# Kernel optimization log

Hardware: AMD Instinct MI355X
Metric: run time of the kernel (lower is better)

## Reference

```python
import jax, jax.numpy as jnp
import numpy as np

# EdMIPS quantizer constants for 2-bit
HWGQ_STEP = 0.538      # hwgq_steps[2]
GAUSS_STEP = 0.996     # gaussian_steps[2]
ABIT = 2
WBIT = 2
BN_EPS = 1e-3


def setup_inputs() -> dict:
    key = jax.random.key(0)
    k1, k2 = jax.random.split(key, 2)
    x = jax.random.normal(k1, (32, 128, 56, 56), jnp.float32)
    gamma = jnp.ones((128,), jnp.float32)
    beta = jnp.zeros((128,), jnp.float32)
    weight = jax.random.normal(k2, (128, 128, 3, 3), jnp.float32) * 0.05
    return {"x": x, "gamma": gamma, "beta": beta, "weight": weight}


def _hwgq(x):
    # HWGQ: clamp to [0, step*(2^abit - 1)], then round to uniform levels.
    lvls = float(2 ** ABIT - 1)
    thr = HWGQ_STEP * lvls
    y = jnp.clip(x, 0.0, thr)
    q = jnp.round(y / HWGQ_STEP) * HWGQ_STEP
    # straight-through estimator: forward = q, backward = d/dy (clip mask)
    return y + jax.lax.stop_gradient(q - y)


def _gauss_quantize(w):
    # step scaled by weight std (detached, torch uses .item()); mid-rise quantizer.
    step = GAUSS_STEP * jax.lax.stop_gradient(jnp.std(w))
    lvls = float(2 ** WBIT) / 2.0
    q = (jnp.round(w / step + 0.5) - 0.5) * step
    thr = (lvls - 0.5) * step
    q = jnp.clip(q, -thr, thr)
    # full straight-through: backward = identity
    return w + jax.lax.stop_gradient(q - w)


def reference(x, gamma, beta, weight):
    # BatchNorm2d (training-mode batch stats, biased variance, eps=0.001)
    mean = jnp.mean(x, axis=(0, 2, 3), keepdims=True)
    var = jnp.var(x, axis=(0, 2, 3), keepdims=True)
    xn = (x - mean) * jax.lax.rsqrt(var + BN_EPS)
    xn = xn * gamma[None, :, None, None] + beta[None, :, None, None]
    # quantized activations and weights, then plain conv (bias=False)
    a = _hwgq(xn)
    qw = _gauss_quantize(weight)
    out = jax.lax.conv_general_dilated(
        a, qw,
        window_strides=(1, 1),
        padding=((1, 1), (1, 1)),
        dimension_numbers=("NCHW", "OIHW", "NCHW"),
    )
    return out  # [32, 128, 56, 56]
```

## Files before the change

kernel.cpp:

```cpp
#include <hip/hip_runtime.h>

typedef int i32x4 __attribute__((ext_vector_type(4)));

#define C_IN 128
#define HW 56
#define PIX 3136
#define NPLANE 401408
#define PROWB 7424
#define APAD_NSTRIDE 430592

static __device__ __forceinline__ void gload_lds16(const void* g, void* l) {
  __builtin_amdgcn_global_load_lds((__attribute__((address_space(1))) unsigned int*)g,
                                   (__attribute__((address_space(3))) unsigned int*)l, 16, 0, 0);
}

__global__ __launch_bounds__(256) void bn_partial_k(const float* __restrict__ x,
                                                    double* __restrict__ part) {
  const int c = blockIdx.x, sl = blockIdx.y;
  const int tid = threadIdx.x;
  double s = 0.0, s2 = 0.0;
  for (int n = sl * 4; n < sl * 4 + 4; ++n) {
    const float4* p = (const float4*)(x + (size_t)(n * C_IN + c) * PIX);
    for (int i = tid; i < PIX / 4; i += 256) {
      float4 v = p[i];
      s  += (double)v.x + (double)v.y + (double)v.z + (double)v.w;
      s2 += (double)v.x * v.x + (double)v.y * v.y + (double)v.z * v.z + (double)v.w * v.w;
    }
  }
  __shared__ double red[8];
  const int lane = tid & 63, wv = tid >> 6;
  for (int off = 32; off; off >>= 1) { s += __shfl_down(s, off); s2 += __shfl_down(s2, off); }
  if (lane == 0) { red[wv * 2] = s; red[wv * 2 + 1] = s2; }
  __syncthreads();
  if (tid == 0) {
    part[(c * 8 + sl) * 2] = red[0] + red[2] + red[4] + red[6];
    part[(c * 8 + sl) * 2 + 1] = red[1] + red[3] + red[5] + red[7];
  }
}

__global__ __launch_bounds__(256) void w_partial_k(const float* __restrict__ w,
                                                   double* __restrict__ part) {
  const int b = blockIdx.x, tid = threadIdx.x;
  double s = 0.0, s2 = 0.0;
  const float4* p = (const float4*)w;
  for (int i = b * 576 + tid; i < (b + 1) * 576; i += 256) {
    float4 v = p[i];
    s  += (double)v.x + (double)v.y + (double)v.z + (double)v.w;
    s2 += (double)v.x * v.x + (double)v.y * v.y + (double)v.z * v.z + (double)v.w * v.w;
  }
  __shared__ double red[8];
  const int lane = tid & 63, wv = tid >> 6;
  for (int off = 32; off; off >>= 1) { s += __shfl_down(s, off); s2 += __shfl_down(s2, off); }
  if (lane == 0) { red[wv * 2] = s; red[wv * 2 + 1] = s2; }
  __syncthreads();
  if (tid == 0) {
    part[b * 2] = red[0] + red[2] + red[4] + red[6];
    part[b * 2 + 1] = red[1] + red[3] + red[5] + red[7];
  }
}

__global__ __launch_bounds__(256) void quant_act_k(const float* __restrict__ x,
                                                   const double* __restrict__ bnpart,
                                                   const float* __restrict__ gamma,
                                                   const float* __restrict__ beta,
                                                   signed char* __restrict__ apad) {
  const int hh = blockIdx.x;
  const int n = blockIdx.y;
  const int tid = threadIdx.x;
  __shared__ float2 aff[128];
  __shared__ __align__(16) signed char lds[58 * 144];
  if (tid < 128) {
    double s = 0.0, s2 = 0.0;
    for (int i = 0; i < 8; ++i) { s += bnpart[(tid * 8 + i) * 2]; s2 += bnpart[(tid * 8 + i) * 2 + 1]; }
    const double mean = s / 100352.0;
    const double var = s2 / 100352.0 - mean * mean;
    const double inv = 1.0 / sqrt(var + 1e-3);
    aff[tid] = make_float2((float)((double)gamma[tid] * inv),
                           (float)((double)beta[tid] - mean * inv * (double)gamma[tid]));
  }
  uint4* lds4 = (uint4*)lds;
  for (int i = tid; i < 58 * 144 / 16; i += 256) lds4[i] = make_uint4(0, 0, 0, 0);
  __syncthreads();
  if (hh >= 1 && hh <= 56) {
    const float* xp = x + (size_t)n * NPLANE + (hh - 1) * HW;
    for (int i = tid; i < C_IN * HW; i += 256) {
      const int w = i % HW, c = i / HW;
      const float v = xp[(size_t)c * PIX + w];
      const float2 af = aff[c];
      const float xn = fmaf(v, af.x, af.y);
      const float y = fminf(fmaxf(xn, 0.f), 1.614f);
      lds[(w + 1) * 144 + c] = (signed char)(int)rintf(y * (1.f / 0.538f));
    }
  }
  __syncthreads();
  signed char* dst = apad + (size_t)n * APAD_NSTRIDE;
  for (int i = tid; i < 58 * 8; i += 256) {
    const int col = i >> 3, c16 = i & 7;
    const int pp = hh * 58 + col;
    *(uint4*)(dst + (((size_t)pp * 128 + c16 * 16) ^ ((pp & 7) << 4))) = lds4[col * 9 + c16];
  }
}

__global__ __launch_bounds__(128) void quant_w_k(const float* __restrict__ w,
                                                 const double* __restrict__ wpart,
                                                 signed char* __restrict__ wq,
                                                 float* __restrict__ stepp) {
  const int oc = blockIdx.x, tid = threadIdx.x;
  __shared__ float steps;
  __shared__ __align__(16) signed char lds[9 * 128];
  if (tid < 64) {
    double s = wpart[tid * 2], s2 = wpart[tid * 2 + 1];
    for (int off = 32; off; off >>= 1) { s += __shfl_down(s, off); s2 += __shfl_down(s2, off); }
    if (tid == 0) {
      const double mean = s / 147456.0;
      const double var = s2 / 147456.0 - mean * mean;
      steps = 0.996f * (float)sqrt(var);
      if (oc == 0) stepp[0] = steps;
    }
  }
  __syncthreads();
  const float step = steps;
  for (int i = tid; i < 1152; i += 128) {
    const int c = i / 9, rs = i % 9;
    const float v = w[(size_t)(oc * C_IN + c) * 9 + rs];
    float t = 2.f * rintf(v / step + 0.5f) - 1.f;
    t = fminf(fmaxf(t, -3.f), 3.f);
    lds[rs * 128 + c] = (signed char)(int)t;
  }
  __syncthreads();
  for (int i = tid; i < 72; i += 128) {
    const int rs = i >> 3, c16 = i & 7;
    *(uint4*)(wq + rs * 16384 + ((oc * 128 + c16 * 16) ^ ((oc & 7) << 4))) =
        *(const uint4*)(lds + rs * 128 + c16 * 16);
  }
}

__global__ __launch_bounds__(256, 2) void conv_k(const signed char* __restrict__ apad,
                                                 const signed char* __restrict__ wq,
                                                 const float* __restrict__ stepp,
                                                 float* __restrict__ out) {
  __shared__ __align__(16) signed char Al[45056];
  __shared__ __align__(16) signed char Wl[2][16384];
  const int rg = blockIdx.x;
  const int n = blockIdx.y;
  const int tid = threadIdx.x;
  const int wv = tid >> 6, lane = tid & 63;
  const int lr = lane & 15, q4 = lane >> 4;
  const int kq = q4 * 16;
  const int ohalf = (wv & 1) * 64;
  const int phalf = (wv >> 1) * 112;

  {
    const signed char* gsrc = apad + (size_t)n * APAD_NSTRIDE + (size_t)(rg * 4) * PROWB;
    for (int i = wv; i < 44; i += 4)
      gload_lds16(gsrc + i * 1024 + lane * 16, Al + i * 1024);
  }
  for (int i = wv; i < 16; i += 4)
    gload_lds16(wq + i * 1024 + lane * 16, &Wl[0][i * 1024]);

  int pbase[7];
#pragma unroll
  for (int pf = 0; pf < 7; ++pf) {
    const int po = phalf + pf * 16 + lr;
    pbase[7 > pf ? pf : 0] = (po / 56) * 58 + po % 56;
  }

  i32x4 acc[7][4];
#pragma unroll
  for (int i = 0; i < 7; ++i)
#pragma unroll
    for (int j = 0; j < 4; ++j) acc[i][j] = (i32x4){0, 0, 0, 0};

  __syncthreads();

  for (int rs = 0; rs < 9; ++rs) {
    if (rs < 8) {
      for (int i = wv; i < 16; i += 4)
        gload_lds16(wq + (rs + 1) * 16384 + i * 1024 + lane * 16, &Wl[(rs + 1) & 1][i * 1024]);
    }
    const int r = rs / 3, s = rs - 3 * r;
    const int poff = r * 58 + s;
    const signed char* Wb = Wl[rs & 1];
#pragma unroll
    for (int k64 = 0; k64 < 2; ++k64) {
      const int kb = k64 * 64 + kq;
      i32x4 wf[4];
#pragma unroll
      for (int of = 0; of < 4; ++of) {
        const int row = ohalf + of * 16 + lr;
        wf[of] = *(const i32x4*)(Wb + row * 128 + (kb ^ ((row & 7) << 4)));
      }
#pragma unroll
      for (int pf = 0; pf < 7; ++pf) {
        const int p = pbase[pf] + poff;
        const i32x4 bf = *(const i32x4*)(Al + p * 128 + (kb ^ ((p & 7) << 4)));
        acc[pf][0] = __builtin_amdgcn_mfma_i32_16x16x64_i8(wf[0], bf, acc[pf][0], 0, 0, 0);
        acc[pf][1] = __builtin_amdgcn_mfma_i32_16x16x64_i8(wf[1], bf, acc[pf][1], 0, 0, 0);
        acc[pf][2] = __builtin_amdgcn_mfma_i32_16x16x64_i8(wf[2], bf, acc[pf][2], 0, 0, 0);
        acc[pf][3] = __builtin_amdgcn_mfma_i32_16x16x64_i8(wf[3], bf, acc[pf][3], 0, 0, 0);
      }
    }
    __syncthreads();
  }

  const float oscale = 0.269f * stepp[0];
  float* outn = out + (size_t)n * NPLANE + (size_t)rg * 224;
#pragma unroll
  for (int pf = 0; pf < 7; ++pf) {
    const int po = phalf + pf * 16 + lr;
    float* op = outn + po;
#pragma unroll
    for (int of = 0; of < 4; ++of) {
      const int oc = ohalf + of * 16 + q4 * 4;
#pragma unroll
      for (int q = 0; q < 4; ++q)
        op[(size_t)(oc + q) * PIX] = (float)acc[pf][of][q] * oscale;
    }
  }
}

extern "C" void kernel_launch(void* const* d_in, const int* in_sizes, int n_in,
                              void* d_out, int out_size, void* d_ws, size_t ws_size,
                              hipStream_t stream) {
  const float* x = (const float*)d_in[0];
  const float* gamma = (const float*)d_in[1];
  const float* beta = (const float*)d_in[2];
  const float* w = (const float*)d_in[3];
  float* out = (float*)d_out;
  char* ws = (char*)d_ws;

  double* bnpart = (double*)(ws);
  double* wpart = (double*)(ws + 16384);
  float* stepp = (float*)(ws + 17408);
  signed char* wq = (signed char*)(ws + 18432);
  signed char* apad = (signed char*)(ws + 196608);

  bn_partial_k<<<dim3(128, 8), 256, 0, stream>>>(x, bnpart);
  w_partial_k<<<64, 256, 0, stream>>>(w, wpart);
  quant_act_k<<<dim3(58, 32), 256, 0, stream>>>(x, bnpart, gamma, beta, apad);
  quant_w_k<<<128, 128, 0, stream>>>(w, wpart, wq, stepp);
  conv_k<<<dim3(14, 32), 256, 0, stream>>>(apad, wq, stepp, out);
}
```

Baseline: 61.73 us.

## Merge stats and quantize kernels, remap conv block order, drop final barrier

Combines the BN-stat and weight-stat reductions into one launch, and the activation and weight quantizers into one launch with an extra grid row for weights. This cuts five kernel launches to three and lets the small weight work overlap with the activation work. The conv grid is flattened and its block index remapped so that neighbouring blocks land on different XCDs, which may change L2 locality for the shared weights and activation rows. The trailing __syncthreads after the last tap is skipped.

Result: faster. 52.84 us (-14.4%).

```diff
diff --git a/kernel.cpp b/kernel.cpp
--- a/kernel.cpp
+++ b/kernel.cpp
@@ -14,14 +14,26 @@
                                    (__attribute__((address_space(3))) unsigned int*)l, 16, 0, 0);
 }
 
-__global__ __launch_bounds__(256) void bn_partial_k(const float* __restrict__ x,
-                                                    double* __restrict__ part) {
-  const int c = blockIdx.x, sl = blockIdx.y;
-  const int tid = threadIdx.x;
+__global__ __launch_bounds__(256) void stats_k(const float* __restrict__ x,
+                                               const float* __restrict__ w,
+                                               double* __restrict__ bnpart,
+                                               double* __restrict__ wpart) {
+  const int b = blockIdx.x, tid = threadIdx.x;
   double s = 0.0, s2 = 0.0;
-  for (int n = sl * 4; n < sl * 4 + 4; ++n) {
-    const float4* p = (const float4*)(x + (size_t)(n * C_IN + c) * PIX);
-    for (int i = tid; i < PIX / 4; i += 256) {
+  if (b < 1024) {
+    const int c = b & 127, sl = b >> 7;
+    for (int n = sl * 4; n < sl * 4 + 4; ++n) {
+      const float4* p = (const float4*)(x + (size_t)(n * C_IN + c) * PIX);
+      for (int i = tid; i < PIX / 4; i += 256) {
+        float4 v = p[i];
+        s  += (double)v.x + (double)v.y + (double)v.z + (double)v.w;
+        s2 += (double)v.x * v.x + (double)v.y * v.y + (double)v.z * v.z + (double)v.w * v.w;
+      }
+    }
+  } else {
+    const int wb = b - 1024;
+    const float4* p = (const float4*)w;
+    for (int i = wb * 576 + tid; i < (wb + 1) * 576; i += 256) {
       float4 v = p[i];
       s  += (double)v.x + (double)v.y + (double)v.z + (double)v.w;
       s2 += (double)v.x * v.x + (double)v.y * v.y + (double)v.z * v.z + (double)v.w * v.w;
@@ -33,40 +45,64 @@
   if (lane == 0) { red[wv * 2] = s; red[wv * 2 + 1] = s2; }
   __syncthreads();
   if (tid == 0) {
-    part[(c * 8 + sl) * 2] = red[0] + red[2] + red[4] + red[6];
-    part[(c * 8 + sl) * 2 + 1] = red[1] + red[3] + red[5] + red[7];
-  }
-}
-
-__global__ __launch_bounds__(256) void w_partial_k(const float* __restrict__ w,
-                                                   double* __restrict__ part) {
-  const int b = blockIdx.x, tid = threadIdx.x;
-  double s = 0.0, s2 = 0.0;
-  const float4* p = (const float4*)w;
-  for (int i = b * 576 + tid; i < (b + 1) * 576; i += 256) {
-    float4 v = p[i];
-    s  += (double)v.x + (double)v.y + (double)v.z + (double)v.w;
-    s2 += (double)v.x * v.x + (double)v.y * v.y + (double)v.z * v.z + (double)v.w * v.w;
-  }
-  __shared__ double red[8];
-  const int lane = tid & 63, wv = tid >> 6;
-  for (int off = 32; off; off >>= 1) { s += __shfl_down(s, off); s2 += __shfl_down(s2, off); }
-  if (lane == 0) { red[wv * 2] = s; red[wv * 2 + 1] = s2; }
-  __syncthreads();
-  if (tid == 0) {
-    part[b * 2] = red[0] + red[2] + red[4] + red[6];
-    part[b * 2 + 1] = red[1] + red[3] + red[5] + red[7];
-  }
-}
-
-__global__ __launch_bounds__(256) void quant_act_k(const float* __restrict__ x,
-                                                   const double* __restrict__ bnpart,
-                                                   const float* __restrict__ gamma,
-                                                   const float* __restrict__ beta,
-                                                   signed char* __restrict__ apad) {
+    double* dst = (b < 1024) ? (bnpart + ((b & 127) * 8 + (b >> 7)) * 2)
+                             : (wpart + (b - 1024) * 2);
+    dst[0] = red[0] + red[2] + red[4] + red[6];
+    dst[1] = red[1] + red[3] + red[5] + red[7];
+  }
+}
+
+__global__ __launch_bounds__(256) void quant_k(const float* __restrict__ x,
+                                               const float* __restrict__ w,
+                                               const float* __restrict__ gamma,
+                                               const float* __restrict__ beta,
+                                               const double* __restrict__ bnpart,
+                                               const double* __restrict__ wpart,
+                                               signed char* __restrict__ apad,
+                                               signed char* __restrict__ wq,
+                                               float* __restrict__ stepp) {
+  const int tid = threadIdx.x;
+  if (blockIdx.y == 32) {
+    const int bx = blockIdx.x;
+    __shared__ float steps;
+    __shared__ __align__(16) signed char wl[3 * 1152];
+    if (tid < 64) {
+      double s = wpart[tid * 2], s2 = wpart[tid * 2 + 1];
+      for (int off = 32; off; off >>= 1) { s += __shfl_down(s, off); s2 += __shfl_down(s2, off); }
+      if (tid == 0) {
+        const double mean = s / 147456.0;
+        const double var = s2 / 147456.0 - mean * mean;
+        steps = 0.996f * (float)sqrt(var);
+        if (bx == 0) stepp[0] = steps;
+      }
+    }
+    __syncthreads();
+    const float step = steps;
+    for (int i = tid; i < 3456; i += 256) {
+      const int oi = i / 1152, rem = i - oi * 1152;
+      const int oc = bx + oi * 58;
+      if (oc < 128) {
+        const int c = rem / 9, rs = rem - c * 9;
+        const float v = w[(size_t)(oc * C_IN + c) * 9 + rs];
+        float t = 2.f * rintf(v / step + 0.5f) - 1.f;
+        t = fminf(fmaxf(t, -3.f), 3.f);
+        wl[oi * 1152 + rs * 128 + c] = (signed char)(int)t;
+      }
+    }
+    __syncthreads();
+    for (int i = tid; i < 216; i += 256) {
+      const int oi = i / 72, rem = i - oi * 72;
+      const int oc = bx + oi * 58;
+      if (oc < 128) {
+        const int rs = rem >> 3, c16 = rem & 7;
+        *(uint4*)(wq + rs * 16384 + ((oc * 128 + c16 * 16) ^ ((oc & 7) << 4))) =
+            *(const uint4*)(wl + oi * 1152 + rs * 128 + c16 * 16);
+      }
+    }
+    return;
+  }
   const int hh = blockIdx.x;
   const int n = blockIdx.y;
-  const int tid = threadIdx.x;
   __shared__ float2 aff[128];
   __shared__ __align__(16) signed char lds[58 * 144];
   if (tid < 128) {
@@ -84,12 +120,12 @@
   if (hh >= 1 && hh <= 56) {
     const float* xp = x + (size_t)n * NPLANE + (hh - 1) * HW;
     for (int i = tid; i < C_IN * HW; i += 256) {
-      const int w = i % HW, c = i / HW;
-      const float v = xp[(size_t)c * PIX + w];
+      const int ww = i % HW, c = i / HW;
+      const float v = xp[(size_t)c * PIX + ww];
       const float2 af = aff[c];
       const float xn = fmaf(v, af.x, af.y);
       const float y = fminf(fmaxf(xn, 0.f), 1.614f);
-      lds[(w + 1) * 144 + c] = (signed char)(int)rintf(y * (1.f / 0.538f));
+      lds[(ww + 1) * 144 + c] = (signed char)(int)rintf(y * (1.f / 0.538f));
     }
   }
   __syncthreads();
@@ -98,40 +134,6 @@
     const int col = i >> 3, c16 = i & 7;
     const int pp = hh * 58 + col;
     *(uint4*)(dst + (((size_t)pp * 128 + c16 * 16) ^ ((pp & 7) << 4))) = lds4[col * 9 + c16];
-  }
-}
-
-__global__ __launch_bounds__(128) void quant_w_k(const float* __restrict__ w,
-                                                 const double* __restrict__ wpart,
-                                                 signed char* __restrict__ wq,
-                                                 float* __restrict__ stepp) {
-  const int oc = blockIdx.x, tid = threadIdx.x;
-  __shared__ float steps;
-  __shared__ __align__(16) signed char lds[9 * 128];
-  if (tid < 64) {
-    double s = wpart[tid * 2], s2 = wpart[tid * 2 + 1];
-    for (int off = 32; off; off >>= 1) { s += __shfl_down(s, off); s2 += __shfl_down(s2, off); }
-    if (tid == 0) {
-      const double mean = s / 147456.0;
-      const double var = s2 / 147456.0 - mean * mean;
-      steps = 0.996f * (float)sqrt(var);
-      if (oc == 0) stepp[0] = steps;
-    }
-  }
-  __syncthreads();
-  const float step = steps;
-  for (int i = tid; i < 1152; i += 128) {
-    const int c = i / 9, rs = i % 9;
-    const float v = w[(size_t)(oc * C_IN + c) * 9 + rs];
-    float t = 2.f * rintf(v / step + 0.5f) - 1.f;
-    t = fminf(fmaxf(t, -3.f), 3.f);
-    lds[rs * 128 + c] = (signed char)(int)t;
-  }
-  __syncthreads();
-  for (int i = tid; i < 72; i += 128) {
-    const int rs = i >> 3, c16 = i & 7;
-    *(uint4*)(wq + rs * 16384 + ((oc * 128 + c16 * 16) ^ ((oc & 7) << 4))) =
-        *(const uint4*)(lds + rs * 128 + c16 * 16);
   }
 }
 
@@ -141,8 +143,10 @@
                                                  float* __restrict__ out) {
   __shared__ __align__(16) signed char Al[45056];
   __shared__ __align__(16) signed char Wl[2][16384];
-  const int rg = blockIdx.x;
-  const int n = blockIdx.y;
+  const int bid = blockIdx.x;
+  const int vid = (bid & 7) * 56 + (bid >> 3);
+  const int n = vid / 14;
+  const int rg = vid - n * 14;
   const int tid = threadIdx.x;
   const int wv = tid >> 6, lane = tid & 63;
   const int lr = lane & 15, q4 = lane >> 4;
@@ -162,7 +166,7 @@
 #pragma unroll
   for (int pf = 0; pf < 7; ++pf) {
     const int po = phalf + pf * 16 + lr;
-    pbase[7 > pf ? pf : 0] = (po / 56) * 58 + po % 56;
+    pbase[pf] = (po / 56) * 58 + po % 56;
   }
 
   i32x4 acc[7][4];
@@ -200,7 +204,7 @@
         acc[pf][3] = __builtin_amdgcn_mfma_i32_16x16x64_i8(wf[3], bf, acc[pf][3], 0, 0, 0);
       }
     }
-    __syncthreads();
+    if (rs < 8) __syncthreads();
   }
 
   const float oscale = 0.269f * stepp[0];
@@ -235,9 +239,7 @@
   signed char* wq = (signed char*)(ws + 18432);
   signed char* apad = (signed char*)(ws + 196608);
 
-  bn_partial_k<<<dim3(128, 8), 256, 0, stream>>>(x, bnpart);
-  w_partial_k<<<64, 256, 0, stream>>>(w, wpart);
-  quant_act_k<<<dim3(58, 32), 256, 0, stream>>>(x, bnpart, gamma, beta, apad);
-  quant_w_k<<<128, 128, 0, stream>>>(w, wpart, wq, stepp);
-  conv_k<<<dim3(14, 32), 256, 0, stream>>>(apad, wq, stepp, out);
-}
+  stats_k<<<1088, 256, 0, stream>>>(x, w, bnpart, wpart);
+  quant_k<<<dim3(58, 33), 256, 0, stream>>>(x, w, gamma, beta, bnpart, wpart, apad, wq, stepp);
+  conv_k<<<448, 256, 0, stream>>>(apad, wq, stepp, out);
+}
```
